# Optimization experiments

Hardware: AMD Instinct MI355X
Metric: run time of the kernel (lower is better)

Reference implementation:

```python
import jax, jax.numpy as jnp
import numpy as np

B, T9, N, C = 2048, 9, 62, 10   # batch, graph_num, node_num, dim_in
TT = 8                           # conv steps t=1..8
D = 62                           # TLSGCN dim_out (== node_num, required by GRU input_size)
ED = 3                           # emb_dim
K = 2                            # link_len
P = 100                          # zigzag persistence-image side
H = 62                           # GRU hidden size (BGI dim_out)


def setup_inputs() -> dict:
    key = jax.random.key(0)
    ks = jax.random.split(key, 12)
    s = 0.1
    return {
        "x": jax.random.normal(ks[0], (B, T9, N, C), jnp.float32),
        "zigzag_PI": jax.random.uniform(ks[1], (B, P, P), dtype=jnp.float32),
        "node_embeddings": jax.random.normal(ks[2], (N, ED), jnp.float32),
        "Wp": jax.random.normal(ks[3], (TT, ED, K, C, D), jnp.float32) * s,
        "bp": jax.random.normal(ks[4], (TT, ED, D), jnp.float32) * s,
        "Tparam": jax.random.normal(ks[5], (TT, T9), jnp.float32),
        "Wz": jax.random.normal(ks[6], (TT, P * P), jnp.float32) * 0.01,
        "W_ih": jax.random.normal(ks[7], (3 * H, D), jnp.float32) * s,
        "W_hh": jax.random.normal(ks[8], (3 * H, H), jnp.float32) * s,
        "b_ih": jnp.zeros((3 * H,), jnp.float32),
        "b_hh": jnp.zeros((3 * H,), jnp.float32),
        "W1": jax.random.normal(ks[9], (256, N), jnp.float32) * s,
        "b1": jnp.zeros((256,), jnp.float32),
        "W2": jax.random.normal(ks[10], (3, 256), jnp.float32) * s,
        "b2": jnp.zeros((3,), jnp.float32),
    }


def reference(x, zigzag_PI, node_embeddings, Wp, bp, Tparam, Wz,
              W_ih, W_hh, b_ih, b_hh, W1, b1, W2, b2):
    # --- TLSGCN graph diffusion conv, vectorized over the 8 per-step modules ---
    A = jax.nn.softmax(jax.nn.relu(node_embeddings @ node_embeddings.T), axis=1)  # [N,N]
    S = jnp.stack([jnp.eye(N, dtype=x.dtype), A], axis=0)                          # [K,N,N]
    w = jnp.einsum('ne,tekco->tnkco', node_embeddings, Wp)                         # [TT,N,K,C,D]
    b = jnp.einsum('ne,teo->tno', node_embeddings, bp)                             # [TT,N,D]
    xg = jnp.einsum('knm,btmc->btknc', S, x[:, 1:, :, :])                          # [B,TT,K,N,C]
    x_gconv = jnp.einsum('btknc,tnkco->btno', xg, w) + b[None]                     # [B,TT,N,D]
    # temporal window: step t attends over its first t frames (window_len = t)
    tmask = jnp.arange(T9)[None, :] < jnp.arange(1, TT + 1)[:, None]               # [TT,T9]
    alpha = jax.nn.softmax(jnp.where(tmask, Tparam, -jnp.inf), axis=1)             # [TT,T9]
    xw = jnp.einsum('bsnc,ts->btnc', x, alpha)                                     # [B,TT,N,C]
    x_wconv = jnp.einsum('btnc,tnco->btno', xw, w[:, :, 0])                        # [B,TT,N,D]
    # zigzag persistence-image topological gate (per step)
    zz = jax.nn.sigmoid(jnp.einsum('bp,tp->bt', zigzag_PI.reshape(B, -1), Wz))     # [B,TT]
    h = zz[:, :, None, None] * x_gconv + x_wconv                                   # [B,TT,N,D]
    h = jnp.where(jnp.isnan(h) | jnp.isinf(h), jnp.zeros((), h.dtype), h)
    # --- shared GRU applied per node: fold nodes into the batch dim ---
    seq = h.transpose(1, 0, 2, 3).reshape(TT, B * N, D)                            # [TT, B*N, D]

    def cell(hprev, xt):
        gi = xt @ W_ih.T + b_ih
        gh = hprev @ W_hh.T + b_hh
        ir, iz, inn = jnp.split(gi, 3, axis=-1)
        hr, hz, hn = jnp.split(gh, 3, axis=-1)
        r = jax.nn.sigmoid(ir + hr)
        zg = jax.nn.sigmoid(iz + hz)
        ng = jnp.tanh(inn + r * hn)
        hnew = (1.0 - zg) * ng + zg * hprev
        return hnew, None

    h0 = jnp.zeros((B * N, H), seq.dtype)
    hT, _ = jax.lax.scan(cell, h0, seq)        # final hidden == output at last step
    out = hT.reshape(B, N, H).sum(axis=2)      # [B, N]
    out = jax.nn.relu(out @ W1.T + b1)         # [B, 256]
    out = jax.nn.relu(out @ W2.T + b2)         # [B, 3]
    return out
```

## Files before the change

### kernel.cpp

```cpp
#include <hip/hip_runtime.h>

typedef unsigned short u16;
typedef unsigned int u32;
typedef _Float16 f16;
typedef __attribute__((ext_vector_type(8))) _Float16 h8v;
typedef __attribute__((ext_vector_type(4))) float f4v;

__device__ __forceinline__ u16 f2h_bits(float f){
  f16 h = (f16)f;
  return __builtin_bit_cast(u16, h);
}
__device__ __forceinline__ float sigmf(float x){
  return __builtin_amdgcn_rcpf(1.f + __expf(-x));
}
__device__ __forceinline__ float tanh_f(float x){
  return 1.f - 2.f*__builtin_amdgcn_rcpf(__expf(2.f*x) + 1.f);
}

__global__ __launch_bounds__(256) void k_pre(
    const float* __restrict__ E, const float* __restrict__ Tp,
    const float* __restrict__ Whh, const float* __restrict__ bih,
    const float* __restrict__ bhh, const float* __restrict__ Wp,
    const float* __restrict__ bp, const float* __restrict__ Wih,
    const float* __restrict__ PI, const float* __restrict__ Wz,
    float* __restrict__ A, float* __restrict__ alpha,
    u16* __restrict__ WhhH, u16* __restrict__ M2, float* __restrict__ zzO)
{
  const int bid = blockIdx.x, tid = threadIdx.x;
  __shared__ float w2s[1240];
  __shared__ float bias[62];
  __shared__ float red[128];

  if (bid < 62){
    if (tid < 64){
      const int n = bid;
      float e0 = E[n*3], e1 = E[n*3+1], e2 = E[n*3+2];
      float s = -1e30f;
      if (tid < 62){
        float d = e0*E[tid*3] + e1*E[tid*3+1] + e2*E[tid*3+2];
        s = d > 0.f ? d : 0.f;
      }
      float mx = s;
      #pragma unroll
      for (int off = 1; off < 64; off <<= 1) mx = fmaxf(mx, __shfl_xor(mx, off));
      float e = (tid < 62) ? __expf(s - mx) : 0.f;
      float sum = e;
      #pragma unroll
      for (int off = 1; off < 64; off <<= 1) sum += __shfl_xor(sum, off);
      if (tid < 62) A[n*62 + tid] = e / sum;
    }
  } else if (bid == 62){
    if (tid < 8){
      int t = tid;
      float mx = -1e30f;
      for (int s = 0; s <= t; ++s) mx = fmaxf(mx, Tp[t*9+s]);
      float sum = 0.f;
      for (int s = 0; s <= t; ++s) sum += __expf(Tp[t*9+s] - mx);
      float inv = 1.f / sum;
      for (int s = 0; s < 9; ++s)
        alpha[t*9+s] = (s <= t) ? __expf(Tp[t*9+s] - mx) * inv : 0.f;
    }
  } else if (bid < 111){
    int i = (bid - 63)*256 + tid;
    if (i < 12288){
      int row = i >> 6, k = i & 63, g = row >> 6, jj = row & 63;
      float vh = 0.f;
      if (jj < 62){
        if (k < 62) vh = Whh[(g*62+jj)*62 + k];
        else if (k == 62) vh = (g < 2) ? (bih[g*62+jj] + bhh[g*62+jj]) : bhh[124+jj];
      }
      WhhH[i] = f2h_bits(vh);
    }
  } else if (bid < 607){
    const int mb = bid - 111;
    const int t = mb / 62, n = mb % 62;
    const float e0 = E[n*3], e1 = E[n*3+1], e2 = E[n*3+2];
    for (int i = tid; i < 1240; i += 256){
      int o = i / 20, k = i % 20, c = k >> 1, kl = k & 1;
      w2s[i] = e0*Wp[(((t*3+0)*2+kl)*10+c)*62 + o]
             + e1*Wp[(((t*3+1)*2+kl)*10+c)*62 + o]
             + e2*Wp[(((t*3+2)*2+kl)*10+c)*62 + o];
    }
    if (tid < 62)
      bias[tid] = e0*bp[(t*3+0)*62+tid] + e1*bp[(t*3+1)*62+tid]
                + e2*bp[(t*3+2)*62+tid];
    __syncthreads();
    for (int i = tid; i < 2304; i += 256){
      int col = i / 12, d = i % 12, g = col >> 6, jj = col & 63;
      unsigned outw = 0;
      if (jj < 62){
        const float* wr = Wih + (g*62+jj)*62;
        if (d < 10){
          int k0 = 2*d;
          float v0 = 0.f, v1 = 0.f;
          for (int o = 0; o < 62; ++o){
            float w = wr[o];
            v0 += w * w2s[o*20 + k0];
            v1 += w * w2s[o*20 + k0 + 1];
          }
          outw = (unsigned)f2h_bits(v0) | ((unsigned)f2h_bits(v1) << 16);
        } else if (d == 10){
          float v0 = 0.f;
          for (int o = 0; o < 62; ++o) v0 += wr[o]*bias[o];
          float v1 = (g == 2) ? bih[124+jj] : 0.f;
          outw = (unsigned)f2h_bits(v0) | ((unsigned)f2h_bits(v1) << 16);
        }
      }
      ((unsigned*)M2)[((size_t)mb*192 + col)*12 + d] = outw;
    }
  } else {
    const int b0 = (bid - 607)*4;
    float acc[32];
    #pragma unroll
    for (int i = 0; i < 32; ++i) acc[i] = 0.f;
    const float4* p0 = (const float4*)(PI + (size_t)(b0+0)*10000);
    const float4* p1 = (const float4*)(PI + (size_t)(b0+1)*10000);
    const float4* p2 = (const float4*)(PI + (size_t)(b0+2)*10000);
    const float4* p3 = (const float4*)(PI + (size_t)(b0+3)*10000);
    const float4* wz4 = (const float4*)Wz;
    for (int p = tid; p < 2500; p += 256){
      float4 x0 = p0[p], x1 = p1[p], x2 = p2[p], x3 = p3[p];
      #pragma unroll
      for (int t = 0; t < 8; ++t){
        float4 w = wz4[t*2500 + p];
        acc[t*4+0] += x0.x*w.x + x0.y*w.y + x0.z*w.z + x0.w*w.w;
        acc[t*4+1] += x1.x*w.x + x1.y*w.y + x1.z*w.z + x1.w*w.w;
        acc[t*4+2] += x2.x*w.x + x2.y*w.y + x2.z*w.z + x2.w*w.w;
        acc[t*4+3] += x3.x*w.x + x3.y*w.y + x3.z*w.z + x3.w*w.w;
      }
    }
    int lane = tid & 63, wid = tid >> 6;
    #pragma unroll
    for (int i = 0; i < 32; ++i){
      float v = acc[i];
      v += __shfl_xor(v, 1);  v += __shfl_xor(v, 2);  v += __shfl_xor(v, 4);
      v += __shfl_xor(v, 8);  v += __shfl_xor(v, 16); v += __shfl_xor(v, 32);
      if (lane == 0) red[i*4 + wid] = v;
    }
    __syncthreads();
    if (tid < 32){
      float s = red[tid*4] + red[tid*4+1] + red[tid*4+2] + red[tid*4+3];
      int t = tid >> 2, bq = tid & 3;
      zzO[t*2048 + b0 + bq] = sigmf(s);
    }
  }
}

__global__ __launch_bounds__(256) void k_u(
    const float* __restrict__ x, const float* __restrict__ A,
    const float* __restrict__ alpha, const float* __restrict__ zz,
    u16* __restrict__ U01)
{
  const int b = blockIdx.x, tid = threadIdx.x;
  __shared__ float xs[5580];
  __shared__ f16 xT[80*72];
  __shared__ f16 A16[64*72];
  __shared__ f16 xg[64*80];
  __shared__ float al[72];
  __shared__ float zzb[8];

  const float* pxb = x + (size_t)b*5580;
  const float4* px4 = (const float4*)pxb;
  for (int i = tid; i < 1395; i += 256) ((float4*)xs)[i] = px4[i];
  for (int i = tid; i < 3844; i += 256){
    int n = i / 62, m = i % 62;
    A16[n*72 + m] = (f16)A[i];
  }
  for (int i = tid; i < 640; i += 256) A16[(i/10)*72 + 62 + (i%10)] = (f16)0.f;
  for (int i = tid; i < 124; i += 256) A16[(62 + i/62)*72 + (i%62)] = (f16)0.f;
  for (int i = tid; i < 4960; i += 256){
    int s1 = i / 620, r = i % 620, m = r / 10, c = r % 10;
    xT[(s1*10 + c)*72 + m] = (f16)pxb[620 + i];
  }
  for (int i = tid; i < 800; i += 256) xT[(i/10)*72 + 62 + (i%10)] = (f16)0.f;
  if (tid < 72) al[tid] = alpha[tid];
  if (tid < 8) zzb[tid] = zz[tid*2048 + b];
  __syncthreads();

  {
    const int w_id = tid >> 6, lane = tid & 63, ln = lane & 15, hi = lane >> 4;
    h8v af0 = *(const h8v*)&A16[(w_id*16 + ln)*72 + hi*8];
    h8v af1 = *(const h8v*)&A16[(w_id*16 + ln)*72 + 32 + hi*8];
    f4v Z4 = {0.f, 0.f, 0.f, 0.f};
    #pragma unroll
    for (int Nt = 0; Nt < 5; ++Nt){
      h8v bf0 = *(const h8v*)&xT[(Nt*16 + ln)*72 + hi*8];
      h8v bf1 = *(const h8v*)&xT[(Nt*16 + ln)*72 + 32 + hi*8];
      f4v acc = __builtin_amdgcn_mfma_f32_16x16x32_f16(af0, bf0, Z4, 0,0,0);
      acc = __builtin_amdgcn_mfma_f32_16x16x32_f16(af1, bf1, acc, 0,0,0);
      #pragma unroll
      for (int rg = 0; rg < 4; ++rg)
        xg[(w_id*16 + hi*4 + rg)*80 + Nt*16 + ln] = (f16)acc[rg];
    }
  }
  __syncthreads();

  const int t = tid >> 5, nq = (tid >> 1) & 15, ch = tid & 1;
  const int n0 = nq*4, c0 = ch*5;
  float alr[9];
  #pragma unroll
  for (int s = 0; s < 9; ++s) alr[s] = al[t*9+s];
  const float z = zzb[t];
  const unsigned zpack = (unsigned)f2h_bits(z) | (0x3C00u << 16);
  #pragma unroll
  for (int i = 0; i < 4; ++i){
    int n = n0 + i;
    if (n < 62){
      unsigned pk[5];
      #pragma unroll
      for (int c = 0; c < 5; ++c){
        int cc = c0 + c;
        float xw = 0.f;
        #pragma unroll
        for (int s = 0; s < 9; ++s) xw += alr[s]*xs[s*620 + n*10 + cc];
        float u0 = z*xs[(t+1)*620 + n*10 + cc] + xw;
        float u1 = z*(float)xg[n*80 + t*10 + cc];
        pk[c] = (unsigned)f2h_bits(u0) | ((unsigned)f2h_bits(u1) << 16);
      }
      unsigned* dst = (unsigned*)(U01 + ((size_t)(t*62 + n)*2048 + b)*24);
      #pragma unroll
      for (int c = 0; c < 5; ++c) dst[c0 + c] = pk[c];
      if (ch == 0) dst[10] = zpack; else dst[11] = 0;
    }
  }
}

__global__ __launch_bounds__(256, 3) void k_gru(
    const u16* __restrict__ U01, const u16* __restrict__ M2,
    const u16* __restrict__ WhhH, float* __restrict__ outSum)
{
  __shared__ f16 Hs[2][32*72];
  __shared__ float red[128];

  const int tid = threadIdx.x;
  int bid = blockIdx.x;
  bid = (bid & 7)*496 + (bid >> 3);
  const int n_idx = bid >> 6;
  const int b0 = (bid & 63) << 5;
  const int lane = tid & 63;
  const int w_id = tid >> 6;
  const int ln = lane & 15;
  const int hi = lane >> 4;
  const int j = w_id*16 + ln;

  h8v whhF[3][2];
  #pragma unroll
  for (int g = 0; g < 3; ++g)
    #pragma unroll
    for (int ks = 0; ks < 2; ++ks)
      whhF[g][ks] = *(const h8v*)(const void*)(WhhH + (g*64 + j)*64 + ks*32 + hi*8);

  for (int i = tid; i < 2304; i += 256){
    f16 v = ((i % 72) == 62) ? (f16)1.f : (f16)0.f;
    Hs[0][i] = v; Hs[1][i] = v;
  }

  auto ldU = [&](int t, int mi)->h8v{
    if (hi == 3) return (h8v){};
    return *(const h8v*)(const void*)(U01 +
        ((size_t)(t*62 + n_idx)*2048 + b0 + mi*16 + ln)*24 + hi*8);
  };
  auto ldM = [&](int t, int g)->h8v{
    if (hi == 3) return (h8v){};
    return *(const h8v*)(const void*)(M2 +
        ((size_t)(t*62 + n_idx)*192 + g*64 + j)*24 + hi*8);
  };

  h8v uA0 = ldU(0,0), uA1 = ldU(0,1);
  h8v uB0, uB1;

  float h_reg[8];
  #pragma unroll
  for (int i = 0; i < 8; ++i) h_reg[i] = 0.f;
  __syncthreads();

  #pragma unroll
  for (int t = 0; t < 8; ++t){
    const int p = t & 1;
    h8v mf0 = ldM(t,0), mf1 = ldM(t,1), mf2 = ldM(t,2);
    if (t < 7){ uB0 = ldU(t+1,0); uB1 = ldU(t+1,1); }

    f4v ar[2], az[2], axn[2], ahn[2];
    #pragma unroll
    for (int mi = 0; mi < 2; ++mi){
      ar[mi] = (f4v){0.f,0.f,0.f,0.f};  az[mi] = (f4v){0.f,0.f,0.f,0.f};
      axn[mi] = (f4v){0.f,0.f,0.f,0.f}; ahn[mi] = (f4v){0.f,0.f,0.f,0.f};
    }
    #pragma unroll
    for (int ks = 0; ks < 2; ++ks)
      #pragma unroll
      for (int mi = 0; mi < 2; ++mi){
        h8v hf = *(const h8v*)&Hs[p][(mi*16 + ln)*72 + ks*32 + hi*8];
        ar[mi]  = __builtin_amdgcn_mfma_f32_16x16x32_f16(hf, whhF[0][ks], ar[mi], 0,0,0);
        az[mi]  = __builtin_amdgcn_mfma_f32_16x16x32_f16(hf, whhF[1][ks], az[mi], 0,0,0);
        ahn[mi] = __builtin_amdgcn_mfma_f32_16x16x32_f16(hf, whhF[2][ks], ahn[mi], 0,0,0);
      }
    ar[0]  = __builtin_amdgcn_mfma_f32_16x16x32_f16(uA0, mf0, ar[0], 0,0,0);
    ar[1]  = __builtin_amdgcn_mfma_f32_16x16x32_f16(uA1, mf0, ar[1], 0,0,0);
    az[0]  = __builtin_amdgcn_mfma_f32_16x16x32_f16(uA0, mf1, az[0], 0,0,0);
    az[1]  = __builtin_amdgcn_mfma_f32_16x16x32_f16(uA1, mf1, az[1], 0,0,0);
    axn[0] = __builtin_amdgcn_mfma_f32_16x16x32_f16(uA0, mf2, axn[0], 0,0,0);
    axn[1] = __builtin_amdgcn_mfma_f32_16x16x32_f16(uA1, mf2, axn[1], 0,0,0);

    const bool last = (t == 7);
    #pragma unroll
    for (int mi = 0; mi < 2; ++mi)
      #pragma unroll
      for (int rg = 0; rg < 4; ++rg){
        float r  = sigmf(ar[mi][rg]);
        float zg = sigmf(az[mi][rg]);
        float ng = tanh_f(axn[mi][rg] + r*ahn[mi][rg]);
        int idx = mi*4 + rg;
        float hnew = ng + zg*(h_reg[idx] - ng);
        h_reg[idx] = hnew;
        if (!last && j < 62)
          Hs[p^1][(mi*16 + hi*4 + rg)*72 + j] = (f16)hnew;
      }
    uA0 = uB0; uA1 = uB1;
    __syncthreads();
  }

  #pragma unroll
  for (int mi = 0; mi < 2; ++mi)
    #pragma unroll
    for (int rg = 0; rg < 4; ++rg){
      float v = (j < 62) ? h_reg[mi*4 + rg] : 0.f;
      v += __shfl_xor(v, 1); v += __shfl_xor(v, 2);
      v += __shfl_xor(v, 4); v += __shfl_xor(v, 8);
      if (ln == 0) red[w_id*32 + mi*16 + hi*4 + rg] = v;
    }
  __syncthreads();
  if (tid < 32)
    outSum[(size_t)n_idx*2048 + b0 + tid] =
        red[tid] + red[32+tid] + red[64+tid] + red[96+tid];
}

__global__ __launch_bounds__(256) void k_mlp(
    const float* __restrict__ outSum,
    const float* __restrict__ W1, const float* __restrict__ b1,
    const float* __restrict__ W2, const float* __restrict__ b2,
    float* __restrict__ out)
{
  const int b = blockIdx.x, tid = threadIdx.x;
  __shared__ float vec[62];
  __shared__ float o1[256];
  if (tid < 62) vec[tid] = outSum[(size_t)tid*2048 + b];
  __syncthreads();
  {
    const float* wr = W1 + tid*62;
    float a = b1[tid];
    #pragma unroll 2
    for (int n = 0; n < 62; ++n) a += wr[n]*vec[n];
    o1[tid] = fmaxf(a, 0.f);
  }
  __syncthreads();
  const int w_id = tid >> 6, lane = tid & 63;
  if (w_id < 3){
    float s = 0.f;
    #pragma unroll
    for (int q = 0; q < 4; ++q){
      int k = q*64 + lane;
      s += o1[k]*W2[w_id*256 + k];
    }
    s += __shfl_xor(s, 1);  s += __shfl_xor(s, 2);  s += __shfl_xor(s, 4);
    s += __shfl_xor(s, 8);  s += __shfl_xor(s, 16); s += __shfl_xor(s, 32);
    if (lane == 0) out[b*3 + w_id] = fmaxf(s + b2[w_id], 0.f);
  }
}

extern "C" void kernel_launch(void* const* d_in, const int* in_sizes, int n_in,
                              void* d_out, int out_size, void* d_ws, size_t ws_size,
                              hipStream_t stream)
{
  const float* x   = (const float*)d_in[0];
  const float* PI  = (const float*)d_in[1];
  const float* E   = (const float*)d_in[2];
  const float* Wp  = (const float*)d_in[3];
  const float* bp  = (const float*)d_in[4];
  const float* Tp  = (const float*)d_in[5];
  const float* Wz  = (const float*)d_in[6];
  const float* Wih = (const float*)d_in[7];
  const float* Whh = (const float*)d_in[8];
  const float* bih = (const float*)d_in[9];
  const float* bhh = (const float*)d_in[10];
  const float* W1  = (const float*)d_in[11];
  const float* b1  = (const float*)d_in[12];
  const float* W2  = (const float*)d_in[13];
  const float* b2  = (const float*)d_in[14];
  float* out = (float*)d_out;

  char* ws = (char*)d_ws;
  size_t off = 0;
  auto take = [&](size_t bytes)->char*{
    char* p = ws + off; off = (off + bytes + 255) & ~(size_t)255; return p;
  };
  float* pA     = (float*)take(3844*4);
  float* palpha = (float*)take(72*4);
  float* pzz    = (float*)take(16384*4);
  u16*   pWhhH  = (u16*)take(12288*2);
  u16*   pM2    = (u16*)take((size_t)496*192*24*2);
  u16*   pU01   = (u16*)take((size_t)496*2048*24*2);
  float* pos    = (float*)take((size_t)126976*4);

  k_pre<<<1119, 256, 0, stream>>>(E, Tp, Whh, bih, bhh, Wp, bp, Wih, PI, Wz,
                                  pA, palpha, pWhhH, pM2, pzz);
  k_u<<<2048, 256, 0, stream>>>(x, pA, palpha, pzz, pU01);
  k_gru<<<3968, 256, 0, stream>>>(pU01, pM2, pWhhH, pos);
  k_mlp<<<2048, 256, 0, stream>>>(pos, W1, b1, W2, b2, out);
}
```

Measured before the change: 190.6 us.

## Precompute padded fp16 adjacency in k_pre and restructure k_u staging and stores

k_pre now writes the softmax adjacency directly as a zero-padded fp16 [64x72] matrix, so k_u loads MFMA A-fragments straight from global memory instead of converting and staging A into LDS per block. k_u stages x once as fp16 in LDS, building both the raw and transposed copies in one pass, which roughly halves LDS footprint and may raise occupancy. The epilogue maps one thread per (t,n) and writes each 48-byte U01 record with three 16-byte vector stores instead of scattered 32-bit stores. The xg row stride is padded to 82 to reduce bank conflicts. The added risk is lower precision in the temporal weighted sum, since it now reads fp16 x values.

```diff
diff --git a/kernel.cpp b/kernel.cpp
--- a/kernel.cpp
+++ b/kernel.cpp
@@ -5,6 +5,7 @@
 typedef _Float16 f16;
 typedef __attribute__((ext_vector_type(8))) _Float16 h8v;
 typedef __attribute__((ext_vector_type(4))) float f4v;
+typedef __attribute__((ext_vector_type(4))) u32 u4v;
 
 __device__ __forceinline__ u16 f2h_bits(float f){
   f16 h = (f16)f;
@@ -23,7 +24,7 @@
     const float* __restrict__ bhh, const float* __restrict__ Wp,
     const float* __restrict__ bp, const float* __restrict__ Wih,
     const float* __restrict__ PI, const float* __restrict__ Wz,
-    float* __restrict__ A, float* __restrict__ alpha,
+    u16* __restrict__ A16G, float* __restrict__ alpha,
     u16* __restrict__ WhhH, u16* __restrict__ M2, float* __restrict__ zzO)
 {
   const int bid = blockIdx.x, tid = threadIdx.x;
@@ -32,8 +33,8 @@
   __shared__ float red[128];
 
   if (bid < 62){
+    const int n = bid;
     if (tid < 64){
-      const int n = bid;
       float e0 = E[n*3], e1 = E[n*3+1], e2 = E[n*3+2];
       float s = -1e30f;
       if (tid < 62){
@@ -47,7 +48,10 @@
       float sum = e;
       #pragma unroll
       for (int off = 1; off < 64; off <<= 1) sum += __shfl_xor(sum, off);
-      if (tid < 62) A[n*62 + tid] = e / sum;
+      if (tid < 62) A16G[n*72 + tid] = f2h_bits(e / sum);
+      else A16G[n*72 + tid] = 0;
+    } else if (tid < 72){
+      A16G[n*72 + tid] = 0;
     }
   } else if (bid == 62){
     if (tid < 8){
@@ -60,6 +64,7 @@
       for (int s = 0; s < 9; ++s)
         alpha[t*9+s] = (s <= t) ? __expf(Tp[t*9+s] - mx) * inv : 0.f;
     }
+    if (tid >= 64 && tid < 208) A16G[62*72 + (tid - 64)] = 0;
   } else if (bid < 111){
     int i = (bid - 63)*256 + tid;
     if (i < 12288){
@@ -147,30 +152,27 @@
 }
 
 __global__ __launch_bounds__(256) void k_u(
-    const float* __restrict__ x, const float* __restrict__ A,
+    const float* __restrict__ x, const u16* __restrict__ A16G,
     const float* __restrict__ alpha, const float* __restrict__ zz,
     u16* __restrict__ U01)
 {
   const int b = blockIdx.x, tid = threadIdx.x;
-  __shared__ float xs[5580];
+  __shared__ f16 xs16[5580];
   __shared__ f16 xT[80*72];
-  __shared__ f16 A16[64*72];
-  __shared__ f16 xg[64*80];
+  __shared__ f16 xg[64*82];
   __shared__ float al[72];
   __shared__ float zzb[8];
 
   const float* pxb = x + (size_t)b*5580;
-  const float4* px4 = (const float4*)pxb;
-  for (int i = tid; i < 1395; i += 256) ((float4*)xs)[i] = px4[i];
-  for (int i = tid; i < 3844; i += 256){
-    int n = i / 62, m = i % 62;
-    A16[n*72 + m] = (f16)A[i];
-  }
-  for (int i = tid; i < 640; i += 256) A16[(i/10)*72 + 62 + (i%10)] = (f16)0.f;
-  for (int i = tid; i < 124; i += 256) A16[(62 + i/62)*72 + (i%62)] = (f16)0.f;
-  for (int i = tid; i < 4960; i += 256){
-    int s1 = i / 620, r = i % 620, m = r / 10, c = r % 10;
-    xT[(s1*10 + c)*72 + m] = (f16)pxb[620 + i];
+  for (int i = tid; i < 5580; i += 256){
+    float v = pxb[i];
+    f16 h = (f16)v;
+    xs16[i] = h;
+    int s = i / 620;
+    if (s >= 1){
+      int r = i % 620, m = r / 10, c = r % 10;
+      xT[((s-1)*10 + c)*72 + m] = h;
+    }
   }
   for (int i = tid; i < 800; i += 256) xT[(i/10)*72 + 62 + (i%10)] = (f16)0.f;
   if (tid < 72) al[tid] = alpha[tid];
@@ -179,8 +181,8 @@
 
   {
     const int w_id = tid >> 6, lane = tid & 63, ln = lane & 15, hi = lane >> 4;
-    h8v af0 = *(const h8v*)&A16[(w_id*16 + ln)*72 + hi*8];
-    h8v af1 = *(const h8v*)&A16[(w_id*16 + ln)*72 + 32 + hi*8];
+    h8v af0 = *(const h8v*)(const void*)(A16G + (w_id*16 + ln)*72 + hi*8);
+    h8v af1 = *(const h8v*)(const void*)(A16G + (w_id*16 + ln)*72 + 32 + hi*8);
     f4v Z4 = {0.f, 0.f, 0.f, 0.f};
     #pragma unroll
     for (int Nt = 0; Nt < 5; ++Nt){
@@ -190,37 +192,36 @@
       acc = __builtin_amdgcn_mfma_f32_16x16x32_f16(af1, bf1, acc, 0,0,0);
       #pragma unroll
       for (int rg = 0; rg < 4; ++rg)
-        xg[(w_id*16 + hi*4 + rg)*80 + Nt*16 + ln] = (f16)acc[rg];
-    }
-  }
-  __syncthreads();
-
-  const int t = tid >> 5, nq = (tid >> 1) & 15, ch = tid & 1;
-  const int n0 = nq*4, c0 = ch*5;
-  float alr[9];
+        xg[(w_id*16 + hi*4 + rg)*82 + Nt*16 + ln] = (f16)acc[rg];
+    }
+  }
+  __syncthreads();
+
   #pragma unroll
-  for (int s = 0; s < 9; ++s) alr[s] = al[t*9+s];
-  const float z = zzb[t];
-  const unsigned zpack = (unsigned)f2h_bits(z) | (0x3C00u << 16);
-  #pragma unroll
-  for (int i = 0; i < 4; ++i){
-    int n = n0 + i;
-    if (n < 62){
-      unsigned pk[5];
-      #pragma unroll
-      for (int c = 0; c < 5; ++c){
-        int cc = c0 + c;
+  for (int r = 0; r < 2; ++r){
+    int idx = r*256 + tid;
+    if (idx < 496){
+      int t = idx / 62, n = idx % 62;
+      float alr[9];
+      #pragma unroll
+      for (int s = 0; s < 9; ++s) alr[s] = al[t*9+s];
+      const float z = zzb[t];
+      u32 d[12];
+      #pragma unroll
+      for (int c = 0; c < 10; ++c){
         float xw = 0.f;
         #pragma unroll
-        for (int s = 0; s < 9; ++s) xw += alr[s]*xs[s*620 + n*10 + cc];
-        float u0 = z*xs[(t+1)*620 + n*10 + cc] + xw;
-        float u1 = z*(float)xg[n*80 + t*10 + cc];
-        pk[c] = (unsigned)f2h_bits(u0) | ((unsigned)f2h_bits(u1) << 16);
-      }
-      unsigned* dst = (unsigned*)(U01 + ((size_t)(t*62 + n)*2048 + b)*24);
-      #pragma unroll
-      for (int c = 0; c < 5; ++c) dst[c0 + c] = pk[c];
-      if (ch == 0) dst[10] = zpack; else dst[11] = 0;
+        for (int s = 0; s < 9; ++s) xw += alr[s]*(float)xs16[s*620 + n*10 + c];
+        float u0 = z*(float)xs16[(t+1)*620 + n*10 + c] + xw;
+        float u1 = z*(float)xg[n*82 + t*10 + c];
+        d[c] = (u32)f2h_bits(u0) | ((u32)f2h_bits(u1) << 16);
+      }
+      d[10] = (u32)f2h_bits(z) | (0x3C00u << 16);
+      d[11] = 0;
+      u4v* dst = (u4v*)(U01 + ((size_t)(t*62 + n)*2048 + b)*24);
+      dst[0] = (u4v){d[0], d[1], d[2], d[3]};
+      dst[1] = (u4v){d[4], d[5], d[6], d[7]};
+      dst[2] = (u4v){d[8], d[9], d[10], d[11]};
     }
   }
 }
@@ -394,7 +395,7 @@
   auto take = [&](size_t bytes)->char*{
     char* p = ws + off; off = (off + bytes + 255) & ~(size_t)255; return p;
   };
-  float* pA     = (float*)take(3844*4);
+  u16*   pA16G  = (u16*)take(4608*2);
   float* palpha = (float*)take(72*4);
   float* pzz    = (float*)take(16384*4);
   u16*   pWhhH  = (u16*)take(12288*2);
@@ -403,8 +404,8 @@
   float* pos    = (float*)take((size_t)126976*4);
 
   k_pre<<<1119, 256, 0, stream>>>(E, Tp, Whh, bih, bhh, Wp, bp, Wih, PI, Wz,
-                                  pA, palpha, pWhhH, pM2, pzz);
-  k_u<<<2048, 256, 0, stream>>>(x, pA, palpha, pzz, pU01);
+                                  pA16G, palpha, pWhhH, pM2, pzz);
+  k_u<<<2048, 256, 0, stream>>>(x, pA16G, palpha, pzz, pU01);
   k_gru<<<3968, 256, 0, stream>>>(pU01, pM2, pWhhH, pos);
   k_mlp<<<2048, 256, 0, stream>>>(pos, W1, b1, W2, b2, out);
 }
```

Result: faster. 181.1 us (-5.0%).
